# Performance work log

Hardware: AMD Instinct MI355X
Metric: run time of the kernel (lower is better)

## Reference

```python
import jax, jax.numpy as jnp
import numpy as np

# Config from init_kwargs
B = 16
CIN = 128
COUT = 256
N = 16        # num_filters
L = 32        # length
K = 3         # kernel_size
KAPPA = 4
STRIDE = 1
PAD = 2
LP = L + PAD  # padded spatial length for FFT


def make_wn():
    # DFT-derived channel-mixing matrix, (cin, d) with d = cout // n
    v = np.arange(CIN)[:, None]
    sr = N * CIN // COUT
    inds = np.arange(CIN)[np.arange(CIN) % sr == 0]
    M = v @ v[inds].T  # (cin, d)
    wn = np.exp((2j * np.pi / CIN) * M) / CIN
    return jnp.asarray(wn.astype(np.complex64))


def setup_inputs() -> dict:
    key = jax.random.key(0)
    k1, k2 = jax.random.split(key)
    x = jax.random.normal(k1, (B, CIN, L, L), dtype=jnp.float32)
    rng = float(np.sqrt(KAPPA / (CIN * K * K)))
    weight = (jax.random.uniform(k2, (N, CIN // KAPPA, K, K), dtype=jnp.float32) - 0.5) * 2.0 * rng
    return {"x": x, "weight": weight}


def reference(x, weight):
    wn = make_wn()  # complex64 (CIN, COUT//N), constant buffer
    # 3D real FFT over (channel, h, w); weight zero-padded from cin//kappa -> cin channels
    x_hat = jnp.fft.rfftn(x, s=(CIN, LP, LP), axes=(-3, -2, -1))          # (B, CIN, LP, LP//2+1)
    w_hat = jnp.fft.rfftn(weight, s=(CIN, LP, LP), axes=(-3, -2, -1))     # (N, CIN, LP, LP//2+1)
    freq = jnp.einsum('bchw,nchw->bnchw', x_hat, w_hat)                   # broadcast, no reduction
    out = jnp.fft.irfftn(freq, s=(LP, LP), axes=(-2, -1))                 # real (B, N, CIN, LP, LP)
    # complex channel mix contracting c -> d; result complex, take real part
    out = jnp.einsum('cd,bnchw->bndhw', wn, out)                          # (B, N, D, LP, LP) complex
    out = out.real[:, :, :, PAD:, PAD:]                                   # (B, N, D, L, L)
    out = jnp.transpose(out, (0, 2, 1, 3, 4))                             # (B, D, N, L, L)
    out = out.reshape(out.shape[0], -1, out.shape[3], out.shape[4])       # (B, COUT, L, L)
    if STRIDE == 2:
        idx = jnp.arange(0, L, 2)
        out = out[:, :, idx, :][:, :, :, idx]
    return out
```

## Files before the change

### kernel.cpp

```cpp
#include <hip/hip_runtime.h>
#include <hip/hip_bf16.h>


typedef __attribute__((ext_vector_type(8))) short short8;
typedef __attribute__((ext_vector_type(4))) float floatx4;

#define NT 512
#define LCH 168
#define SROWS 34
#define XSROW (SROWS * LCH)

template<int D, bool DUP>
__device__ __forceinline__ void compute_d(const char* basep, const short8 af[9],
                                          float* opbase) {
    floatx4 a0 = {0.f,0.f,0.f,0.f}, a1 = {0.f,0.f,0.f,0.f};
    floatx4 b0 = {0.f,0.f,0.f,0.f}, b1 = {0.f,0.f,0.f,0.f};
#pragma unroll
    for (int u = 0; u < 3; ++u)
#pragma unroll
        for (int v = 0; v < 3; ++v) {
            const int t = u * 3 + v;
            const short8 ba = *(const short8*)(basep +
                ((u * SROWS + v) * LCH + 8 * (8 + D)) * 2);
            if (t & 1) a1 = __builtin_amdgcn_mfma_f32_16x16x32_bf16(af[t], ba, a1, 0, 0, 0);
            else       a0 = __builtin_amdgcn_mfma_f32_16x16x32_bf16(af[t], ba, a0, 0, 0, 0);
            if (!DUP) {
                const short8 bb = *(const short8*)(basep +
                    ((u * SROWS + v) * LCH + 8 * (8 - D)) * 2);
                if (t & 1) b1 = __builtin_amdgcn_mfma_f32_16x16x32_bf16(af[t], bb, b1, 0, 0, 0);
                else       b0 = __builtin_amdgcn_mfma_f32_16x16x32_bf16(af[t], bb, b0, 0, 0, 0);
            }
        }
    floatx4 acc = a0 + a1;
    if (DUP) acc = acc + acc;
    else     acc = acc + (b0 + b1);
    float* op = opbase + D * 16384;
    op[0]    = acc.x;
    op[1024] = acc.y;
    op[2048] = acc.z;
    op[3072] = acc.w;
    if (D >= 1 && D <= 7) {
        float* op2 = opbase + (16 - D) * 16384;
        op2[0]    = acc.x;
        op2[1024] = acc.y;
        op2[2048] = acc.z;
        op2[3072] = acc.w;
    }
}

__global__ __launch_bounds__(NT, 2)
void fconv_mfma(const float* __restrict__ x,
                const float* __restrict__ wgt,
                float* __restrict__ out) {
    __shared__ __align__(16) short xs[4 * XSROW];
    __shared__ __align__(16) short wf[9 * 640];

    const int rq   = blockIdx.x;
    const int b    = blockIdx.y;
    const int r0   = rq * 2;
    const int tid  = threadIdx.x;
    const int lane = tid & 63;
    const int wv   = tid >> 6;

    {
        const int n  = tid >> 5;
        const int c2 = tid & 31;
        const float* wb = wgt + (size_t)(n * 32 + c2) * 9;
        const int pos = n * 40 + (c2 & 24) + (7 - (c2 & 7));
#pragma unroll
        for (int k = 0; k < 9; ++k) {
            __hip_bfloat16 h = __float2bfloat16(0.5f * wb[k]);
            wf[(8 - k) * 640 + pos] = __builtin_bit_cast(short, h);
        }
    }

    const float* xb_base = x + ((size_t)b << 17);
#pragma unroll
    for (int it = 0; it < 5; ++it) {
        const int idx  = wv * 320 + it * 64 + lane;
        const int col  = idx & 31;
        const int rest = idx >> 5;
        const int lrow = rest & 3;
        const int oL   = rest >> 2;
        const int grow = r0 + lrow;
        short8 g;
        if (grow < 32) {
            float v[8];
#pragma unroll
            for (int j = 0; j < 8; ++j) {
                const int m = (oL * 8 + j - 95) & 127;
                v[j] = xb_base[((m << 5) + grow) * 32 + col];
            }
            union { __hip_bfloat162 h2[4]; short8 s8; } u;
#pragma unroll
            for (int p = 0; p < 4; ++p)
                u.h2[p] = __float22bfloat162_rn(make_float2(v[2 * p], v[2 * p + 1]));
            g = u.s8;
        } else {
            g = short8{0, 0, 0, 0, 0, 0, 0, 0};
        }
        *(short8*)&xs[(lrow * SROWS + col) * LCH + oL * 8] = g;
    }
    if (tid < 160) {
        const int oL   = tid % 20;
        const int rem  = tid / 20;
        const int lrow = rem >> 1;
        const int col  = 32 + (rem & 1);
        short8 z = {0, 0, 0, 0, 0, 0, 0, 0};
        *(short8*)&xs[(lrow * SROWS + col) * LCH + oL * 8] = z;
    }

    __syncthreads();

    const int n = lane & 15;
    const int q = lane >> 4;
    short8 af[9];
#pragma unroll
    for (int t = 0; t < 9; ++t)
        af[t] = *(const short8*)&wf[t * 640 + n * 40 + q * 8];

    const int tile = wv & 3;
    const int lr   = tile >> 1;
    const int sh   = tile & 1;
    const int s0   = sh << 4;
    const int dg   = wv >> 2;

    const char* basep = (const char*)xs +
        ((lr * SROWS + s0 + n) * LCH + 8 * (3 - q)) * 2;
    float* opbase = out + ((size_t)((b * 256 + q * 4) * 32 + (r0 + lr)) << 5) + s0 + n;

    if (dg == 0) {
        compute_d<0, true >(basep, af, opbase);
        compute_d<2, false>(basep, af, opbase);
        compute_d<4, false>(basep, af, opbase);
        compute_d<6, false>(basep, af, opbase);
        compute_d<8, true >(basep, af, opbase);
    } else {
        compute_d<1, false>(basep, af, opbase);
        compute_d<3, false>(basep, af, opbase);
        compute_d<5, false>(basep, af, opbase);
        compute_d<7, false>(basep, af, opbase);
    }
}

extern "C" void kernel_launch(void* const* d_in, const int* in_sizes, int n_in,
                              void* d_out, int out_size, void* d_ws, size_t ws_size,
                              hipStream_t stream) {
    const float* x   = (const float*)d_in[0];
    const float* wgt = (const float*)d_in[1];
    float* out = (float*)d_out;
    (void)in_sizes; (void)n_in; (void)out_size; (void)d_ws; (void)ws_size;

    fconv_mfma<<<dim3(16, 16), dim3(NT), 0, stream>>>(x, wgt, out);
}
```

Measured before the change: 70.47 us.

## Process one output row per block, doubling grid and rebalancing wave work

Each block now handles a single output row instead of two, staging 3 input rows into shared memory instead of 4, and the grid grows from 16x16 to 32x16 blocks. The eight waves are redistributed as two column halves by four d-groups, so each wave does 2-3 d-values rather than 4-5. Launch bounds now request 4 blocks per SM. The aim is more parallelism across CUs and better occupancy, at the cost of more redundant global input loads (3 rows staged per output row instead of 2) and the weight staging being repeated in twice as many blocks.

Result: no change. 71.24 us (+1.1%).

```diff
diff --git a/kernel.cpp b/kernel.cpp
--- a/kernel.cpp
+++ b/kernel.cpp
@@ -48,16 +48,15 @@
     }
 }
 
-__global__ __launch_bounds__(NT, 2)
+__global__ __launch_bounds__(NT, 4)
 void fconv_mfma(const float* __restrict__ x,
                 const float* __restrict__ wgt,
                 float* __restrict__ out) {
-    __shared__ __align__(16) short xs[4 * XSROW];
+    __shared__ __align__(16) short xs[3 * XSROW];
     __shared__ __align__(16) short wf[9 * 640];
 
-    const int rq   = blockIdx.x;
+    const int r    = blockIdx.x;
     const int b    = blockIdx.y;
-    const int r0   = rq * 2;
     const int tid  = threadIdx.x;
     const int lane = tid & 63;
     const int wv   = tid >> 6;
@@ -76,32 +75,34 @@
 
     const float* xb_base = x + ((size_t)b << 17);
 #pragma unroll
-    for (int it = 0; it < 5; ++it) {
-        const int idx  = wv * 320 + it * 64 + lane;
-        const int col  = idx & 31;
-        const int rest = idx >> 5;
-        const int lrow = rest & 3;
-        const int oL   = rest >> 2;
-        const int grow = r0 + lrow;
-        short8 g;
-        if (grow < 32) {
-            float v[8];
+    for (int it = 0; it < 4; ++it) {
+        const int idx = it * NT + tid;
+        if (idx < 1920) {
+            const int col  = idx & 31;
+            const int rest = idx >> 5;
+            const int oL   = rest / 3;
+            const int lrow = rest - oL * 3;
+            const int grow = r + lrow;
+            short8 g;
+            if (grow < 32) {
+                float v[8];
 #pragma unroll
-            for (int j = 0; j < 8; ++j) {
-                const int m = (oL * 8 + j - 95) & 127;
-                v[j] = xb_base[((m << 5) + grow) * 32 + col];
+                for (int j = 0; j < 8; ++j) {
+                    const int m = (oL * 8 + j - 95) & 127;
+                    v[j] = xb_base[((m << 5) + grow) * 32 + col];
+                }
+                union { __hip_bfloat162 h2[4]; short8 s8; } u;
+#pragma unroll
+                for (int p = 0; p < 4; ++p)
+                    u.h2[p] = __float22bfloat162_rn(make_float2(v[2 * p], v[2 * p + 1]));
+                g = u.s8;
+            } else {
+                g = short8{0, 0, 0, 0, 0, 0, 0, 0};
             }
-            union { __hip_bfloat162 h2[4]; short8 s8; } u;
-#pragma unroll
-            for (int p = 0; p < 4; ++p)
-                u.h2[p] = __float22bfloat162_rn(make_float2(v[2 * p], v[2 * p + 1]));
-            g = u.s8;
-        } else {
-            g = short8{0, 0, 0, 0, 0, 0, 0, 0};
+            *(short8*)&xs[(lrow * SROWS + col) * LCH + oL * 8] = g;
         }
-        *(short8*)&xs[(lrow * SROWS + col) * LCH + oL * 8] = g;
     }
-    if (tid < 160) {
+    if (tid < 120) {
         const int oL   = tid % 20;
         const int rem  = tid / 20;
         const int lrow = rem >> 1;
@@ -119,26 +120,25 @@
     for (int t = 0; t < 9; ++t)
         af[t] = *(const short8*)&wf[t * 640 + n * 40 + q * 8];
 
-    const int tile = wv & 3;
-    const int lr   = tile >> 1;
-    const int sh   = tile & 1;
-    const int s0   = sh << 4;
-    const int dg   = wv >> 2;
+    const int half = wv & 1;
+    const int dq   = wv >> 1;
+    const int s0   = half << 4;
 
-    const char* basep = (const char*)xs +
-        ((lr * SROWS + s0 + n) * LCH + 8 * (3 - q)) * 2;
-    float* opbase = out + ((size_t)((b * 256 + q * 4) * 32 + (r0 + lr)) << 5) + s0 + n;
+    const char* basep = (const char*)xs + ((s0 + n) * LCH + 8 * (3 - q)) * 2;
+    float* opbase = out + ((size_t)((b * 256 + q * 4) * 32 + r) << 5) + s0 + n;
 
-    if (dg == 0) {
+    if (dq == 0) {
         compute_d<0, true >(basep, af, opbase);
+        compute_d<4, false>(basep, af, opbase);
+        compute_d<8, true >(basep, af, opbase);
+    } else if (dq == 1) {
         compute_d<2, false>(basep, af, opbase);
-        compute_d<4, false>(basep, af, opbase);
         compute_d<6, false>(basep, af, opbase);
-        compute_d<8, true >(basep, af, opbase);
+    } else if (dq == 2) {
+        compute_d<1, false>(basep, af, opbase);
+        compute_d<5, false>(basep, af, opbase);
     } else {
-        compute_d<1, false>(basep, af, opbase);
         compute_d<3, false>(basep, af, opbase);
-        compute_d<5, false>(basep, af, opbase);
         compute_d<7, false>(basep, af, opbase);
     }
 }
@@ -151,5 +151,5 @@
     float* out = (float*)d_out;
     (void)in_sizes; (void)n_in; (void)out_size; (void)d_ws; (void)ws_size;
 
-    fconv_mfma<<<dim3(16, 16), dim3(NT), 0, stream>>>(x, wgt, out);
+    fconv_mfma<<<dim3(32, 16), dim3(NT), 0, stream>>>(x, wgt, out);
 }
```
